# Kernel tuning notes

Hardware: AMD Instinct MI355X
Metric: run time of the kernel (lower is better)

Reference implementation:

```python
import jax, jax.numpy as jnp
import numpy as np

B = 4            # scenes
N = 100000       # points per scene
BN = B * N
M = 200000       # occupied target voxels
C_IMG = 64       # img_feat_dim
C_3D = 32        # INIT_DIM (3D feature width at p1 scale)
COORD_MAX = 256  # voxel grid extent per axis


def setup_inputs() -> dict:
    key = jax.random.key(0)
    k1, k2, k3, k4, k5, k6 = jax.random.split(key, 6)
    # batched voxel coords: col0 = batch idx, cols1:4 = xyz voxel coords
    bcol = jax.random.randint(k1, (M, 1), 0, B, dtype=jnp.int32)
    xyz = jax.random.randint(k2, (M, 3), 0, COORD_MAX, dtype=jnp.int32)
    tgt_coords = jnp.concatenate([bcol, xyz], axis=1)  # (M,4)
    # each point maps onto some target voxel (torch code asserts full validity)
    pts_idx = jax.random.randint(k3, (BN,), 0, M, dtype=jnp.int32)
    pfeat = jax.random.normal(k4, (BN, C_IMG), dtype=jnp.float32)
    tgt_feats = jax.random.normal(k5, (M, C_3D), dtype=jnp.float32)
    W_fuse = jax.random.normal(k6, (C_3D + C_IMG, C_3D), dtype=jnp.float32) * 0.05
    b_fuse = jnp.zeros((C_3D,), dtype=jnp.float32)
    return {"pfeat": pfeat, "tgt_feats": tgt_feats, "W_fuse": W_fuse,
            "b_fuse": b_fuse, "tgt_coords": tgt_coords, "pts_idx": pts_idx}


def reference(pfeat, tgt_feats, W_fuse, b_fuse, tgt_coords, pts_idx):
    # point voxel coords (stride-snapped in torch; identity here since points map to voxels)
    pts_coords = tgt_coords[pts_idx]                              # (BN,4)
    # --- key packing (mirrors _pack_keys with shift-to-nonnegative) ---
    xyz_all = jnp.concatenate([pts_coords[:, 1:], tgt_coords[:, 1:]], axis=0)
    shift = jnp.maximum(-xyz_all.min(axis=0), 0)
    pts_xyz = pts_coords[:, 1:] + shift
    tgt_xyz = tgt_coords[:, 1:] + shift
    max_xyz = jnp.maximum(pts_xyz.max(axis=0), tgt_xyz.max(axis=0))
    mx, my, mz = max_xyz[0] + 1, max_xyz[1] + 1, max_xyz[2] + 1

    def pack(b, xyz):
        return ((b * mx + xyz[:, 0]) * my + xyz[:, 1]) * mz + xyz[:, 2]

    pts_key = pack(pts_coords[:, 0], pts_xyz)                     # (BN,)
    tgt_key = pack(tgt_coords[:, 0], tgt_xyz)                     # (M,)
    # --- sort target keys, binary-search point keys (torch.sort + searchsorted) ---
    order = jnp.argsort(tgt_key)
    tgt_key_sorted = tgt_key[order]
    pos = jnp.minimum(jnp.searchsorted(tgt_key_sorted, pts_key), M - 1)
    tgt_idx = order[pos]                                          # (BN,) voxel each point lands in
    # --- scatter-mean of 2D point features into voxels (_scatter_mean) ---
    sums = jax.ops.segment_sum(pfeat, tgt_idx, num_segments=M)    # (M,C_IMG)
    cnt = jax.ops.segment_sum(jnp.ones((pfeat.shape[0], 1), pfeat.dtype),
                              tgt_idx, num_segments=M)            # (M,1)
    img_feat_u = sums / jnp.maximum(cnt, 1.0)
    # --- ME.cat + 1x1 MinkowskiConvolution fuse == concat + matmul ---
    fused = jnp.concatenate([tgt_feats, img_feat_u], axis=1)      # (M, C_3D+C_IMG)
    return fused @ W_fuse + b_fuse                                # (M, C_3D)
```

## Files before the change

### kernel.cpp

```cpp
#include <hip/hip_runtime.h>

#define HBITS 19
#define HSIZE (1u << HBITS)
#define HMASK (HSIZE - 1u)
#define EMPTY_KEY 0xFFFFFFFFu
#define SLOTS 8

__device__ __forceinline__ unsigned hash_key(unsigned k) {
    return (k * 2654435761u) >> (32 - HBITS);
}

__device__ __forceinline__ unsigned pack_key(int4 c) {
    return ((unsigned)c.x << 24) | ((unsigned)c.y << 16) |
           ((unsigned)c.z << 8) | (unsigned)c.w;
}

__global__ __launch_bounds__(256)
void build_hash(const int4* __restrict__ tgt_coords, int M,
                uint2* __restrict__ htab) {
    int v = blockIdx.x * blockDim.x + threadIdx.x;
    if (v >= M) return;
    unsigned key = pack_key(tgt_coords[v]);
    unsigned h = hash_key(key);
    while (true) {
        unsigned prev = atomicCAS(&htab[h].x, EMPTY_KEY, key);
        if (prev == EMPTY_KEY || prev == key) {
            atomicMin(&htab[h].y, (unsigned)v);
            break;
        }
        h = (h + 1u) & HMASK;
    }
}

__global__ __launch_bounds__(256)
void canonize(const int4* __restrict__ tgt_coords,
              const uint2* __restrict__ htab, int M,
              int* __restrict__ canon) {
    int v = blockIdx.x * blockDim.x + threadIdx.x;
    if (v >= M) return;
    unsigned key = pack_key(tgt_coords[v]);
    unsigned h = hash_key(key);
    uint2 e = htab[h];
    while (e.x != key) { h = (h + 1u) & HMASK; e = htab[h]; }
    canon[v] = (int)e.y;
}

__global__ __launch_bounds__(256)
void fill_slots(const int* __restrict__ pts_idx,
                const int* __restrict__ canon,
                int BN,
                int* __restrict__ cnt,
                int* __restrict__ slotbuf,
                int* __restrict__ ohead,
                int* __restrict__ nxt) {
    int p = blockIdx.x * blockDim.x + threadIdx.x;
    if (p >= BN) return;
    int c = canon[pts_idx[p]];
    int idx = atomicAdd(&cnt[c], 1) + 1;
    if (idx < SLOTS) slotbuf[c * SLOTS + idx] = p;
    else             nxt[p] = atomicExch(&ohead[c], p);
}

#define VOXB 64
#define XSTR 98
__global__ __launch_bounds__(256, 4)
void gather_fuse(const float2* __restrict__ pf2,
                 const float* __restrict__ tgtf,
                 const int* __restrict__ cnt,
                 const int4* __restrict__ slot4,
                 const int* __restrict__ ohead,
                 const int* __restrict__ nxt,
                 const float* __restrict__ W,
                 const float* __restrict__ bias,
                 int M,
                 float* __restrict__ out) {
    __shared__ __align__(16) float xs[VOXB][XSTR];
    __shared__ int scnt[VOXB];
    __shared__ __align__(16) int4 sslot[VOXB * 2];

    int t = threadIdx.x;
    int vbase = blockIdx.x * VOXB;

    if (t < VOXB) {
        int v = vbase + t;
        scnt[t] = (v < M) ? cnt[v] : -1;
    }
    if (t < VOXB * 2) {
        int j = vbase * 2 + t;
        sslot[t] = (j < M * 2) ? slot4[j] : make_int4(0, 0, 0, 0);
    }
    __syncthreads();

    int grp = t >> 5;
    int g   = t & 31;

    for (int pp = 0; pp < VOXB / 8; ++pp) {
        int vb = pp * 8 + grp;
        int v  = vbase + vb;
        if (v < M) {
            int n = scnt[vb] + 1;
            int4 sa = sslot[vb * 2];
            int4 sb = sslot[vb * 2 + 1];
            float2 f0 = {0,0}, f1 = {0,0}, f2 = {0,0}, f3 = {0,0};
            float2 f4 = {0,0}, f5 = {0,0}, f6 = {0,0}, f7 = {0,0};
            if (n > 0) f0 = pf2[(size_t)sa.x * 32 + g];
            if (n > 1) f1 = pf2[(size_t)sa.y * 32 + g];
            if (n > 2) f2 = pf2[(size_t)sa.z * 32 + g];
            if (n > 3) f3 = pf2[(size_t)sa.w * 32 + g];
            if (n > 4) f4 = pf2[(size_t)sb.x * 32 + g];
            if (n > 5) f5 = pf2[(size_t)sb.y * 32 + g];
            if (n > 6) f6 = pf2[(size_t)sb.z * 32 + g];
            if (n > 7) f7 = pf2[(size_t)sb.w * 32 + g];
            float sx = ((f0.x + f1.x) + (f2.x + f3.x)) + ((f4.x + f5.x) + (f6.x + f7.x));
            float sy = ((f0.y + f1.y) + (f2.y + f3.y)) + ((f4.y + f5.y) + (f6.y + f7.y));
            if (n > SLOTS) {
                int p = ohead[v];
                while (p >= 0) {
                    float2 f = pf2[(size_t)p * 32 + g];
                    sx += f.x; sy += f.y;
                    p = nxt[p];
                }
            }
            float inv = 1.0f / fmaxf((float)n, 1.0f);
            xs[vb][g] = tgtf[(size_t)v * 32 + g];
            *reinterpret_cast<float2*>(&xs[vb][32 + 2 * g]) =
                make_float2(sx * inv, sy * inv);
        }
    }

    __syncthreads();

    int vb2 = t & (VOXB - 1);
    int ocb = __builtin_amdgcn_readfirstlane((t >> 6) << 3);
    int v2  = vbase + vb2;
    if (v2 < M) {
        float acc[8];
#pragma unroll
        for (int j = 0; j < 8; ++j) acc[j] = bias[ocb + j];

#pragma unroll 4
        for (int k4 = 0; k4 < 24; ++k4) {
            float2 xa = *reinterpret_cast<const float2*>(&xs[vb2][k4 * 4]);
            float2 xb = *reinterpret_cast<const float2*>(&xs[vb2][k4 * 4 + 2]);
            const float* w0 = W + (k4 * 4 + 0) * 32 + ocb;
            const float* w1 = W + (k4 * 4 + 1) * 32 + ocb;
            const float* w2 = W + (k4 * 4 + 2) * 32 + ocb;
            const float* w3 = W + (k4 * 4 + 3) * 32 + ocb;
#pragma unroll
            for (int j = 0; j < 8; ++j) {
                acc[j] = fmaf(xa.x, w0[j], acc[j]);
                acc[j] = fmaf(xa.y, w1[j], acc[j]);
                acc[j] = fmaf(xb.x, w2[j], acc[j]);
                acc[j] = fmaf(xb.y, w3[j], acc[j]);
            }
        }

        float4* o = reinterpret_cast<float4*>(out + (size_t)v2 * 32 + ocb);
        o[0] = make_float4(acc[0], acc[1], acc[2], acc[3]);
        o[1] = make_float4(acc[4], acc[5], acc[6], acc[7]);
    }
}

extern "C" void kernel_launch(void* const* d_in, const int* in_sizes, int n_in,
                              void* d_out, int out_size, void* d_ws, size_t ws_size,
                              hipStream_t stream) {
    const float* pfeat      = (const float*)d_in[0];
    const float* tgt_feats  = (const float*)d_in[1];
    const float* W_fuse     = (const float*)d_in[2];
    const float* b_fuse     = (const float*)d_in[3];
    const int*   tgt_coords = (const int*)d_in[4];
    const int*   pts_idx    = (const int*)d_in[5];
    float* out = (float*)d_out;

    const int M  = in_sizes[4] / 4;
    const int BN = in_sizes[5];

    char* ws = (char*)d_ws;
    uint2* htab    = (uint2*)ws;
    size_t off = (size_t)HSIZE * 8;
    int*   cnt     = (int*)(ws + off);              off += (size_t)M * 4;
    int*   ohead   = (int*)(ws + off);              off += (size_t)M * 4;
    int*   canon   = (int*)(ws + off);              off += (size_t)M * 4;
    int*   slotbuf = (int*)(ws + off);              off += (size_t)M * SLOTS * 4;
    int*   nxt     = (int*)(ws + off);

    size_t ff_bytes = (size_t)HSIZE * 8 + (size_t)M * 8;
    hipMemsetAsync(htab, 0xFF, ff_bytes, stream);

    const int TB = 256;
    build_hash<<<(M + TB - 1) / TB, TB, 0, stream>>>(
        (const int4*)tgt_coords, M, htab);
    canonize<<<(M + TB - 1) / TB, TB, 0, stream>>>(
        (const int4*)tgt_coords, htab, M, canon);
    fill_slots<<<(BN + TB - 1) / TB, TB, 0, stream>>>(
        pts_idx, canon, BN, cnt, slotbuf, ohead, nxt);
    gather_fuse<<<(M + VOXB - 1) / VOXB, TB, 0, stream>>>(
        (const float2*)pfeat, tgt_feats, cnt, (const int4*)slotbuf, ohead, nxt,
        W_fuse, b_fuse, M, out);
}
```

Baseline: 269.4 us.

## Compact per-block point worklist and scatter-add features into shared memory

The gather phase used to give each voxel to one 32-lane group, which then issued up to eight predicated loads; groups with few points sat idle. Now each block builds a compacted worklist of valid (voxel, point) pairs in LDS using a ballot and prefix count. The eight groups walk that list with four loads in flight and accumulate into the shared feature tile with LDS float atomics. The mean division moves into the matmul loop, and target features are loaded cooperatively with float2 loads. The costs are LDS atomic contention, an extra barrier and a larger shared footprint, which may reduce occupancy.

```diff
diff --git a/kernel.cpp b/kernel.cpp
--- a/kernel.cpp
+++ b/kernel.cpp
@@ -67,7 +67,7 @@
 void gather_fuse(const float2* __restrict__ pf2,
                  const float* __restrict__ tgtf,
                  const int* __restrict__ cnt,
-                 const int4* __restrict__ slot4,
+                 const int* __restrict__ slotbuf,
                  const int* __restrict__ ohead,
                  const int* __restrict__ nxt,
                  const float* __restrict__ W,
@@ -76,70 +76,110 @@
                  float* __restrict__ out) {
     __shared__ __align__(16) float xs[VOXB][XSTR];
     __shared__ int scnt[VOXB];
-    __shared__ __align__(16) int4 sslot[VOXB * 2];
+    __shared__ int wl[VOXB * SLOTS];
+    __shared__ int wcnt;
 
     int t = threadIdx.x;
+    int lane = t & 63;
     int vbase = blockIdx.x * VOXB;
 
+    if (t == 0) wcnt = 0;
     if (t < VOXB) {
         int v = vbase + t;
         scnt[t] = (v < M) ? cnt[v] : -1;
     }
-    if (t < VOXB * 2) {
-        int j = vbase * 2 + t;
-        sslot[t] = (j < M * 2) ? slot4[j] : make_int4(0, 0, 0, 0);
+#pragma unroll
+    for (int k = t; k < VOXB * 32; k += 256) {
+        int vb = k >> 5, col = 32 + (k & 31) * 2;
+        *reinterpret_cast<float2*>(&xs[vb][col]) = make_float2(0.f, 0.f);
+    }
+    {
+        const float2* tg2 = reinterpret_cast<const float2*>(tgtf);
+#pragma unroll
+        for (int k = t; k < VOXB * 16; k += 256) {
+            int vb = k >> 4, idx = k & 15;
+            int v = vbase + vb;
+            float2 val = (v < M) ? tg2[(size_t)v * 16 + idx]
+                                 : make_float2(0.f, 0.f);
+            *reinterpret_cast<float2*>(&xs[vb][idx * 2]) = val;
+        }
+    }
+    __syncthreads();
+
+#pragma unroll
+    for (int rnd = 0; rnd < 2; ++rnd) {
+        int c = t + rnd * 256;
+        int vb = c >> 3;
+        int slot = c & 7;
+        bool valid = (slot <= scnt[vb]);
+        int p = 0;
+        if (valid) p = slotbuf[(size_t)vbase * SLOTS + c];
+        unsigned long long mask = __ballot(valid);
+        int tot = __popcll(mask);
+        int prefix = __popcll(mask & ((1ull << lane) - 1ull));
+        int base = 0;
+        if (lane == 0 && tot > 0) base = atomicAdd(&wcnt, tot);
+        base = __shfl(base, 0);
+        if (valid) wl[base + prefix] = (vb << 19) | p;
     }
     __syncthreads();
 
     int grp = t >> 5;
     int g   = t & 31;
-
-    for (int pp = 0; pp < VOXB / 8; ++pp) {
-        int vb = pp * 8 + grp;
-        int v  = vbase + vb;
-        if (v < M) {
-            int n = scnt[vb] + 1;
-            int4 sa = sslot[vb * 2];
-            int4 sb = sslot[vb * 2 + 1];
-            float2 f0 = {0,0}, f1 = {0,0}, f2 = {0,0}, f3 = {0,0};
-            float2 f4 = {0,0}, f5 = {0,0}, f6 = {0,0}, f7 = {0,0};
-            if (n > 0) f0 = pf2[(size_t)sa.x * 32 + g];
-            if (n > 1) f1 = pf2[(size_t)sa.y * 32 + g];
-            if (n > 2) f2 = pf2[(size_t)sa.z * 32 + g];
-            if (n > 3) f3 = pf2[(size_t)sa.w * 32 + g];
-            if (n > 4) f4 = pf2[(size_t)sb.x * 32 + g];
-            if (n > 5) f5 = pf2[(size_t)sb.y * 32 + g];
-            if (n > 6) f6 = pf2[(size_t)sb.z * 32 + g];
-            if (n > 7) f7 = pf2[(size_t)sb.w * 32 + g];
-            float sx = ((f0.x + f1.x) + (f2.x + f3.x)) + ((f4.x + f5.x) + (f6.x + f7.x));
-            float sy = ((f0.y + f1.y) + (f2.y + f3.y)) + ((f4.y + f5.y) + (f6.y + f7.y));
-            if (n > SLOTS) {
-                int p = ohead[v];
-                while (p >= 0) {
-                    float2 f = pf2[(size_t)p * 32 + g];
-                    sx += f.x; sy += f.y;
-                    p = nxt[p];
-                }
+    int nit = wcnt;
+
+    int i = grp;
+    for (; i + 24 < nit; i += 32) {
+        int it0 = wl[i];
+        int it1 = wl[i + 8];
+        int it2 = wl[i + 16];
+        int it3 = wl[i + 24];
+        float2 f0 = pf2[(size_t)(it0 & 0x7FFFF) * 32 + g];
+        float2 f1 = pf2[(size_t)(it1 & 0x7FFFF) * 32 + g];
+        float2 f2 = pf2[(size_t)(it2 & 0x7FFFF) * 32 + g];
+        float2 f3 = pf2[(size_t)(it3 & 0x7FFFF) * 32 + g];
+        float* r0 = &xs[it0 >> 19][32 + 2 * g];
+        float* r1 = &xs[it1 >> 19][32 + 2 * g];
+        float* r2 = &xs[it2 >> 19][32 + 2 * g];
+        float* r3 = &xs[it3 >> 19][32 + 2 * g];
+        atomicAdd(r0, f0.x); atomicAdd(r0 + 1, f0.y);
+        atomicAdd(r1, f1.x); atomicAdd(r1 + 1, f1.y);
+        atomicAdd(r2, f2.x); atomicAdd(r2 + 1, f2.y);
+        atomicAdd(r3, f3.x); atomicAdd(r3 + 1, f3.y);
+    }
+    for (; i < nit; i += 8) {
+        int it = wl[i];
+        float2 f = pf2[(size_t)(it & 0x7FFFF) * 32 + g];
+        float* r = &xs[it >> 19][32 + 2 * g];
+        atomicAdd(r, f.x); atomicAdd(r + 1, f.y);
+    }
+
+    for (int vb = grp; vb < VOXB; vb += 8) {
+        if (scnt[vb] + 1 > SLOTS) {
+            int p = ohead[vbase + vb];
+            float sx = 0.f, sy = 0.f;
+            while (p >= 0) {
+                float2 f = pf2[(size_t)p * 32 + g];
+                sx += f.x; sy += f.y;
+                p = nxt[p];
             }
-            float inv = 1.0f / fmaxf((float)n, 1.0f);
-            xs[vb][g] = tgtf[(size_t)v * 32 + g];
-            *reinterpret_cast<float2*>(&xs[vb][32 + 2 * g]) =
-                make_float2(sx * inv, sy * inv);
-        }
-    }
-
+            float* r = &xs[vb][32 + 2 * g];
+            atomicAdd(r, sx); atomicAdd(r + 1, sy);
+        }
+    }
     __syncthreads();
 
     int vb2 = t & (VOXB - 1);
     int ocb = __builtin_amdgcn_readfirstlane((t >> 6) << 3);
     int v2  = vbase + vb2;
     if (v2 < M) {
+        float inv = 1.0f / fmaxf((float)(scnt[vb2] + 1), 1.0f);
         float acc[8];
 #pragma unroll
         for (int j = 0; j < 8; ++j) acc[j] = bias[ocb + j];
 
 #pragma unroll 4
-        for (int k4 = 0; k4 < 24; ++k4) {
+        for (int k4 = 0; k4 < 8; ++k4) {
             float2 xa = *reinterpret_cast<const float2*>(&xs[vb2][k4 * 4]);
             float2 xb = *reinterpret_cast<const float2*>(&xs[vb2][k4 * 4 + 2]);
             const float* w0 = W + (k4 * 4 + 0) * 32 + ocb;
@@ -152,6 +192,24 @@
                 acc[j] = fmaf(xa.y, w1[j], acc[j]);
                 acc[j] = fmaf(xb.x, w2[j], acc[j]);
                 acc[j] = fmaf(xb.y, w3[j], acc[j]);
+            }
+        }
+#pragma unroll 4
+        for (int k4 = 8; k4 < 24; ++k4) {
+            float2 xa = *reinterpret_cast<const float2*>(&xs[vb2][k4 * 4]);
+            float2 xb = *reinterpret_cast<const float2*>(&xs[vb2][k4 * 4 + 2]);
+            float m0 = xa.x * inv, m1 = xa.y * inv;
+            float m2 = xb.x * inv, m3 = xb.y * inv;
+            const float* w0 = W + (k4 * 4 + 0) * 32 + ocb;
+            const float* w1 = W + (k4 * 4 + 1) * 32 + ocb;
+            const float* w2 = W + (k4 * 4 + 2) * 32 + ocb;
+            const float* w3 = W + (k4 * 4 + 3) * 32 + ocb;
+#pragma unroll
+            for (int j = 0; j < 8; ++j) {
+                acc[j] = fmaf(m0, w0[j], acc[j]);
+                acc[j] = fmaf(m1, w1[j], acc[j]);
+                acc[j] = fmaf(m2, w2[j], acc[j]);
+                acc[j] = fmaf(m3, w3[j], acc[j]);
             }
         }
 
@@ -195,6 +253,6 @@
     fill_slots<<<(BN + TB - 1) / TB, TB, 0, stream>>>(
         pts_idx, canon, BN, cnt, slotbuf, ohead, nxt);
     gather_fuse<<<(M + VOXB - 1) / VOXB, TB, 0, stream>>>(
-        (const float2*)pfeat, tgt_feats, cnt, (const int4*)slotbuf, ohead, nxt,
+        (const float2*)pfeat, tgt_feats, cnt, slotbuf, ohead, nxt,
         W_fuse, b_fuse, M, out);
 }
```

Result: slower. 354.2 us (+31.5%).
